# Performance work log

Measured on AMD Instinct MI355X. Metric: run time of the kernel, lower is better.

The kernel has to match this reference:

```python
import jax, jax.numpy as jnp
import numpy as np

BN_EPS = 1e-5
SG = jax.lax.stop_gradient


def _silu(z):
    return z * jax.nn.sigmoid(z)


def _binary_activation(x):
    # forward value = sign(x); backward goes through piecewise quadratic out3 (STE)
    out1 = jnp.where(x < -1, -1.0, x * x + 2 * x)
    out2 = jnp.where(x < 0, out1, -x * x + 2 * x)
    out3 = jnp.where(x < 1, out2, 1.0)
    return SG(jnp.sign(x)) - SG(out3) + out3


def _binarize_weight(w):
    # per-output-channel scaling factor * sign(w), STE through clipped weights
    sf = SG(jnp.mean(jnp.abs(w), axis=(1, 2, 3), keepdims=True))  # [O,1,1,1]
    cw = jnp.clip(w, -1.0, 1.0)
    return SG(sf * jnp.sign(w)) - SG(cw) + cw


def _conv3x3_s2(x, w, b):
    y = jax.lax.conv_general_dilated(
        x, w, window_strides=(2, 2), padding=((1, 1), (1, 1)),
        dimension_numbers=("NCHW", "OIHW", "NCHW"))
    return y + b[None, :, None, None]


def _batchnorm_train(x, gamma, beta):
    # training-mode BN: batch statistics over (N,H,W), biased variance
    mean = jnp.mean(x, axis=(0, 2, 3), keepdims=True)
    var = jnp.mean((x - mean) ** 2, axis=(0, 2, 3), keepdims=True)
    xhat = (x - mean) * jax.lax.rsqrt(var + BN_EPS)
    return xhat * gamma[None, :, None, None] + beta[None, :, None, None]


def _learnable_bias(x, emb, w, b):
    # bias = zero_module(linear)(SiLU(emb)) broadcast over H,W
    bias = _silu(emb) @ w.T + b  # [B, C]
    return x + bias[:, :, None, None]


def _avgpool2(x):
    B, C, H, W = x.shape
    return x.reshape(B, C, H // 2, 2, W // 2, 2).mean(axis=(3, 5))


def setup_inputs() -> dict:
    key = jax.random.key(0)
    ks = jax.random.split(key, 16)
    B, Cin, P, E, H, W = 32, 128, 256, 512, 64, 64
    scalor = P // Cin  # 2
    inp = {
        "x": jax.random.normal(ks[0], (B, Cin, H, W), jnp.float32),
        "emb": jax.random.normal(ks[1], (B, E), jnp.float32),
        "m1_w": jax.random.normal(ks[2], (Cin, E), jnp.float32) * 0.02,
        "m1_b": jnp.zeros((Cin,), jnp.float32),
        "conv_w": jax.random.uniform(ks[3], (scalor, Cin, Cin, 3, 3), jnp.float32, -1.0, 1.0) * 0.1,
        "conv_b": jax.random.normal(ks[4], (scalor, Cin), jnp.float32) * 0.01,
        "bn_g": jnp.ones((scalor, Cin), jnp.float32),
        "bn_b": jnp.zeros((scalor, Cin), jnp.float32),
        "m2_w": jax.random.normal(ks[5], (P, E), jnp.float32) * 0.02,
        "m2_b": jnp.zeros((P,), jnp.float32),
        "prelu_a": jnp.full((P,), 0.25, jnp.float32),
        "m3_w": jax.random.normal(ks[6], (P, E), jnp.float32) * 0.02,
        "m3_b": jnp.zeros((P,), jnp.float32),
    }
    return inp


def reference(x, emb, m1_w, m1_b, conv_w, conv_b, bn_g, bn_b,
              m2_w, m2_b, prelu_a, m3_w, m3_b):
    scalor = conv_w.shape[0]
    out = _learnable_bias(x, emb, m1_w, m1_b)
    out = _binary_activation(out)
    xp = _avgpool2(x)  # residual, [B,Cin,H/2,W/2]
    out_list = []
    for i in range(scalor):
        bw = _binarize_weight(conv_w[i])
        y = _conv3x3_s2(out, bw, conv_b[i])
        y = _batchnorm_train(y, bn_g[i], bn_b[i])
        out_list.append(y + xp)
    o = jnp.concatenate(out_list, axis=1)  # [B, planes, H/2, W/2]
    o = _learnable_bias(o, emb, m2_w, m2_b)
    a = prelu_a[None, :, None, None]
    o = jnp.where(o > 0, o, a * o)  # PReLU per channel
    o = _learnable_bias(o, emb, m3_w, m3_b)
    return o
```

## Files before the change

kernel.cpp:

```cpp
#include <hip/hip_runtime.h>
#include <cstdint>
#include <cstddef>

#define B_  32
#define CIN 128
#define P_  256
#define E_  512
#define H_  64
#define W_  64
#define HO  32
#define WO  32

__global__ void k_bw(const float* __restrict__ emb,
                     const float* __restrict__ m1_w, const float* __restrict__ m1_b,
                     const float* __restrict__ m2_w, const float* __restrict__ m2_b,
                     const float* __restrict__ m3_w, const float* __restrict__ m3_b,
                     const float* __restrict__ conv_w,
                     float* __restrict__ b1, float* __restrict__ b2, float* __restrict__ b3,
                     float* __restrict__ sf, unsigned int* __restrict__ wbits,
                     float* __restrict__ s1, float* __restrict__ s2) {
    int bid = blockIdx.x;
    int tid = threadIdx.x;
    int wave = tid >> 6, lane = tid & 63;

    if (bid < B_ * 160) {
        int n = bid / 160, rg = bid % 160;
        int row = rg * 4 + wave;
        const float* sp = emb + n * E_;
        const float* wrow; float bias; float* dst;
        if (row < CIN)            { wrow = m1_w + (size_t)row * E_;          bias = m1_b[row]; dst = b1 + n * CIN + row; }
        else if (row < CIN + P_)  { int c = row - CIN;      wrow = m2_w + (size_t)c * E_; bias = m2_b[c]; dst = b2 + n * P_ + c; }
        else                      { int c = row - CIN - P_; wrow = m3_w + (size_t)c * E_; bias = m3_b[c]; dst = b3 + n * P_ + c; }
        float acc = 0.f;
        #pragma unroll
        for (int j = 0; j < 8; j++) {
            int k = j * 64 + lane;
            float e = sp[k];
            acc += (e / (1.f + expf(-e))) * wrow[k];
        }
        #pragma unroll
        for (int off = 32; off > 0; off >>= 1) acc += __shfl_down(acc, off);
        if (lane == 0) *dst = acc + bias;
        return;
    }

    int base = (bid - B_ * 160) * 2;
    int oc = base + (wave >> 1);
    int iw = wave & 1;
    int i  = iw * 64 + lane;
    if (lane == 0 && iw == 0) { s1[oc] = 0.f; s2[oc] = 0.f; }
    const float* wp = conv_w + ((size_t)oc * CIN + i) * 9;
    float w[9]; float s = 0.f;
    #pragma unroll
    for (int t = 0; t < 9; t++) { w[t] = wp[t]; s += fabsf(w[t]); }
    #pragma unroll
    for (int t = 0; t < 9; t++) {
        unsigned long long m = __ballot(w[t] < 0.f);
        if (lane == 0) {
            wbits[oc * 36 + t * 4 + iw * 2 + 0] = (unsigned int)(m & 0xffffffffull);
            wbits[oc * 36 + t * 4 + iw * 2 + 1] = (unsigned int)(m >> 32);
        }
    }
    #pragma unroll
    for (int off = 32; off > 0; off >>= 1) s += __shfl_down(s, off);
    __shared__ float sred[4];
    if (lane == 0) sred[wave] = s;
    __syncthreads();
    if (tid == 0)        sf[base]     = (sred[0] + sred[1]) / 1152.f;
    else if (tid == 128) sf[base + 1] = (sred[2] + sred[3]) / 1152.f;
}

__global__ void k_prep(const float* __restrict__ x, const float* __restrict__ b1,
                       unsigned int* __restrict__ abits, float* __restrict__ xpool) {
    __shared__ float sb1[CIN];
    int n = blockIdx.x >> 5, h2 = blockIdx.x & 31;
    int tid = threadIdx.x;
    for (int i = tid; i < CIN; i += 256) sb1[i] = b1[n * CIN + i];
    __syncthreads();

    int pix = tid >> 1, half = tid & 1;
    int h = 2 * h2 + (pix >> 6), w = pix & 63;
    const float* xp = x + ((size_t)n * CIN + half * 64) * (H_ * W_) + (size_t)h * W_ + w;
    unsigned int wds[2];
    #pragma unroll
    for (int wd = 0; wd < 2; wd++) {
        unsigned int m = 0;
        #pragma unroll
        for (int b = 0; b < 32; b++) {
            float v = xp[(size_t)(wd * 32 + b) * (H_ * W_)] + sb1[half * 64 + wd * 32 + b];
            m |= (v < 0.f ? 1u : 0u) << b;
        }
        wds[wd] = m;
    }
    ((uint2*)abits)[((size_t)n * 4096 + (size_t)h * 64 + w) * 2 + half] = make_uint2(wds[0], wds[1]);

    for (int idx = tid; idx < CIN * WO; idx += 256) {
        int c = idx >> 5, w2 = idx & 31;
        const float* p = x + ((size_t)n * CIN + c) * (H_ * W_) + (size_t)(2 * h2) * W_ + 2 * w2;
        float2 a = *(const float2*)p;
        float2 b = *(const float2*)(p + W_);
        xpool[((size_t)n * CIN + c) * (HO * WO) + h2 * WO + w2] = 0.25f * (a.x + a.y + b.x + b.y);
    }
}

__global__ void __launch_bounds__(256, 4) k_convstat(const unsigned int* __restrict__ abits,
                                                     const unsigned int* __restrict__ wbits,
                                                     short* __restrict__ y16,
                                                     float* __restrict__ s1, float* __restrict__ s2) {
    __shared__ int red1[32][33], red2[32][33];
    int bid = blockIdx.x;
    int strip = bid & 3, ocg = (bid >> 2) & 7, n = bid >> 5;
    int tid = threadIdx.x;
    int wave = tid >> 6, lane = tid & 63;
    int oh = strip * 8 + (tid >> 5), ow = tid & 31;

    const uint4* asrc = ((const uint4*)abits) + ((size_t)n << 12);
    uint4 img[9]; int vmask = 0;
    #pragma unroll
    for (int kh = 0; kh < 3; kh++) {
        #pragma unroll
        for (int kw = 0; kw < 3; kw++) {
            int t = kh * 3 + kw;
            int r = 2 * oh - 1 + kh, c = 2 * ow - 1 + kw;
            bool v = (unsigned)r < 64u && (unsigned)c < 64u;
            img[t] = v ? asrc[r * 64 + c] : make_uint4(0u, 0u, 0u, 0u);
            vmask |= (v ? 1 : 0) << t;
        }
    }
    int base128 = 128 * __popc(vmask);

    const uint4* wp = ((const uint4*)wbits) + (size_t)ocg * 32 * 9;
    short* yp = y16 + (((size_t)n * P_ + ocg * 32) << 10) + strip * 256 + tid;
    #pragma unroll 4
    for (int o = 0; o < 32; o++) {
        int popsum = 0;
        #pragma unroll
        for (int t = 0; t < 9; t++) {
            uint4 a = img[t];
            uint4 w = wp[o * 9 + t];
            int p = __popc(a.x ^ w.x) + __popc(a.y ^ w.y) +
                    __popc(a.z ^ w.z) + __popc(a.w ^ w.w);
            popsum += ((vmask >> t) & 1) ? p : 0;
        }
        int s = base128 - 2 * popsum;
        yp[(size_t)o << 10] = (short)s;
        int vs = s, v2 = s * s;
        vs += __shfl_down(vs, 32); v2 += __shfl_down(v2, 32);
        vs += __shfl_down(vs, 16); v2 += __shfl_down(v2, 16);
        vs += __shfl_down(vs, 8);  v2 += __shfl_down(v2, 8);
        if (lane < 8) { red1[o][wave * 8 + lane] = vs; red2[o][wave * 8 + lane] = v2; }
    }
    __syncthreads();
    if (tid < 64) {
        int o = tid & 31;
        int a = 0;
        if (tid < 32) {
            #pragma unroll
            for (int p = 0; p < 32; p++) a += red1[o][p];
            atomicAdd(s1 + ocg * 32 + o, (float)a);
        } else {
            #pragma unroll
            for (int p = 0; p < 32; p++) a += red2[o][p];
            atomicAdd(s2 + ocg * 32 + o, (float)a);
        }
    }
}

__global__ void k_epi(const short* __restrict__ y16, const float* __restrict__ xpool,
                      const float* __restrict__ sf,
                      const float* __restrict__ s1, const float* __restrict__ s2,
                      const float* __restrict__ bn_g, const float* __restrict__ bn_b,
                      const float* __restrict__ b2, const float* __restrict__ b3,
                      const float* __restrict__ prelu_a, float* __restrict__ out) {
    int i4 = blockIdx.x * blockDim.x + threadIdx.x;
    int pix4 = i4 & 255;
    int c = (i4 >> 8) & 255;
    int n = i4 >> 16;
    short4 yv = ((const short4*)y16)[i4];
    float4 xv = ((const float4*)xpool)[((n * CIN + (c & 127)) << 8) + pix4];
    const float inv = 1.f / (B_ * HO * WO);
    float sc = sf[c];
    float m = sc * s1[c] * inv;
    float var = fmaf(-m, m, sc * sc * s2[c] * inv);
    float r = rsqrtf(var + 1e-5f) * bn_g[c];
    float add0 = bn_b[c] + b2[n * P_ + c];
    float a = prelu_a[c];
    float b3v = b3[n * P_ + c];
    float o0 = (sc * (float)yv.x - m) * r + add0 + xv.x; o0 = (o0 > 0.f ? o0 : a * o0) + b3v;
    float o1 = (sc * (float)yv.y - m) * r + add0 + xv.y; o1 = (o1 > 0.f ? o1 : a * o1) + b3v;
    float o2 = (sc * (float)yv.z - m) * r + add0 + xv.z; o2 = (o2 > 0.f ? o2 : a * o2) + b3v;
    float o3 = (sc * (float)yv.w - m) * r + add0 + xv.w; o3 = (o3 > 0.f ? o3 : a * o3) + b3v;
    ((float4*)out)[i4] = make_float4(o0, o1, o2, o3);
}

extern "C" void kernel_launch(void* const* d_in, const int* in_sizes, int n_in,
                              void* d_out, int out_size, void* d_ws, size_t ws_size,
                              hipStream_t stream) {
    const float* x      = (const float*)d_in[0];
    const float* emb    = (const float*)d_in[1];
    const float* m1_w   = (const float*)d_in[2];
    const float* m1_b   = (const float*)d_in[3];
    const float* conv_w = (const float*)d_in[4];
    const float* bn_g   = (const float*)d_in[6];
    const float* bn_b   = (const float*)d_in[7];
    const float* m2_w   = (const float*)d_in[8];
    const float* m2_b   = (const float*)d_in[9];
    const float* prelu_a= (const float*)d_in[10];
    const float* m3_w   = (const float*)d_in[11];
    const float* m3_b   = (const float*)d_in[12];

    float* out = (float*)d_out;

    float* wsf = (float*)d_ws;
    float* b1    = wsf;
    float* b2    = wsf + 4096;
    float* b3    = wsf + 12288;
    float* sf    = wsf + 20480;
    float* s1    = wsf + 20736;
    float* s2    = wsf + 20992;
    unsigned int* wbits = (unsigned int*)(wsf + 21248);
    unsigned int* abits = (unsigned int*)(wsf + 30464);
    float* xpool = wsf + 554752;
    short* y16   = (short*)(wsf + 4749056 + 16384);

    k_bw      <<<B_ * 160 + P_ / 2, 256, 0, stream>>>(emb, m1_w, m1_b, m2_w, m2_b, m3_w, m3_b,
                                                      conv_w, b1, b2, b3, sf, wbits, s1, s2);
    k_prep    <<<B_ * 32, 256, 0, stream>>>(x, b1, abits, xpool);
    k_convstat<<<B_ * 32, 256, 0, stream>>>(abits, wbits, y16, s1, s2);
    k_epi     <<<(B_ * P_ * HO * WO) / (4 * 256), 256, 0, stream>>>(y16, xpool, sf, s1, s2,
                                                                    bn_g, bn_b, b2, b3, prelu_a, out);
}
```

Baseline: 190.9 us.

## Pad binarized activation image and correct borders with precomputed weight sums

The packed activation bits are stored with a one-pixel zero border (pitch 65), so the XNOR-popcount conv loads its 3x3 taps without bounds checks or validity masks. Boundary outputs are fixed with per-channel corrections for the top row, left column and corner, computed in the weight-binarization kernel from sign counts. The conv kernel also launches twice as many blocks, each handling 16 output channels instead of 32, with a higher occupancy hint. This trades extra per-output correction loads and more atomics for less branch and select work in the inner loop and more parallelism.

```diff
diff --git a/kernel.cpp b/kernel.cpp
--- a/kernel.cpp
+++ b/kernel.cpp
@@ -11,6 +11,9 @@
 #define HO  32
 #define WO  32
 
+#define APITCH 65
+#define APIX   4225
+
 __global__ void k_bw(const float* __restrict__ emb,
                      const float* __restrict__ m1_w, const float* __restrict__ m1_b,
                      const float* __restrict__ m2_w, const float* __restrict__ m2_b,
@@ -18,6 +21,7 @@
                      const float* __restrict__ conv_w,
                      float* __restrict__ b1, float* __restrict__ b2, float* __restrict__ b3,
                      float* __restrict__ sf, unsigned int* __restrict__ wbits,
+                     int* __restrict__ cwrow, int* __restrict__ cwcol, int* __restrict__ cw0,
                      float* __restrict__ s1, float* __restrict__ s2) {
     int bid = blockIdx.x;
     int tid = threadIdx.x;
@@ -51,11 +55,13 @@
     if (lane == 0 && iw == 0) { s1[oc] = 0.f; s2[oc] = 0.f; }
     const float* wp = conv_w + ((size_t)oc * CIN + i) * 9;
     float w[9]; float s = 0.f;
+    int pc[9];
     #pragma unroll
     for (int t = 0; t < 9; t++) { w[t] = wp[t]; s += fabsf(w[t]); }
     #pragma unroll
     for (int t = 0; t < 9; t++) {
         unsigned long long m = __ballot(w[t] < 0.f);
+        pc[t] = __popcll(m);
         if (lane == 0) {
             wbits[oc * 36 + t * 4 + iw * 2 + 0] = (unsigned int)(m & 0xffffffffull);
             wbits[oc * 36 + t * 4 + iw * 2 + 1] = (unsigned int)(m >> 32);
@@ -64,10 +70,30 @@
     #pragma unroll
     for (int off = 32; off > 0; off >>= 1) s += __shfl_down(s, off);
     __shared__ float sred[4];
-    if (lane == 0) sred[wave] = s;
+    __shared__ int spc[4][9];
+    if (lane == 0) {
+        sred[wave] = s;
+        #pragma unroll
+        for (int t = 0; t < 9; t++) spc[wave][t] = pc[t];
+    }
     __syncthreads();
-    if (tid == 0)        sf[base]     = (sred[0] + sred[1]) / 1152.f;
-    else if (tid == 128) sf[base + 1] = (sred[2] + sred[3]) / 1152.f;
+    if (tid == 0) {
+        sf[base] = (sred[0] + sred[1]) / 1152.f;
+        int c_[9];
+        #pragma unroll
+        for (int t = 0; t < 9; t++) c_[t] = spc[0][t] + spc[1][t];
+        cwrow[base] = 384 - 2 * (c_[0] + c_[1] + c_[2]);
+        cwcol[base] = 384 - 2 * (c_[0] + c_[3] + c_[6]);
+        cw0[base]   = 128 - 2 * c_[0];
+    } else if (tid == 128) {
+        sf[base + 1] = (sred[2] + sred[3]) / 1152.f;
+        int c_[9];
+        #pragma unroll
+        for (int t = 0; t < 9; t++) c_[t] = spc[2][t] + spc[3][t];
+        cwrow[base + 1] = 384 - 2 * (c_[0] + c_[1] + c_[2]);
+        cwcol[base + 1] = 384 - 2 * (c_[0] + c_[3] + c_[6]);
+        cw0[base + 1]   = 128 - 2 * c_[0];
+    }
 }
 
 __global__ void k_prep(const float* __restrict__ x, const float* __restrict__ b1,
@@ -78,6 +104,14 @@
     for (int i = tid; i < CIN; i += 256) sb1[i] = b1[n * CIN + i];
     __syncthreads();
 
+    if (h2 == 0) {
+        for (int i = tid; i < 129; i += 256) {
+            size_t idx = (i < 65) ? ((size_t)n * APIX + i)
+                                  : ((size_t)n * APIX + (size_t)(i - 64) * APITCH);
+            ((uint4*)abits)[idx] = make_uint4(0u, 0u, 0u, 0u);
+        }
+    }
+
     int pix = tid >> 1, half = tid & 1;
     int h = 2 * h2 + (pix >> 6), w = pix & 63;
     const float* xp = x + ((size_t)n * CIN + half * 64) * (H_ * W_) + (size_t)h * W_ + w;
@@ -92,7 +126,8 @@
         }
         wds[wd] = m;
     }
-    ((uint2*)abits)[((size_t)n * 4096 + (size_t)h * 64 + w) * 2 + half] = make_uint2(wds[0], wds[1]);
+    ((uint2*)abits)[((size_t)n * APIX + (size_t)(h + 1) * APITCH + (w + 1)) * 2 + half] =
+        make_uint2(wds[0], wds[1]);
 
     for (int idx = tid; idx < CIN * WO; idx += 256) {
         int c = idx >> 5, w2 = idx & 31;
@@ -103,46 +138,48 @@
     }
 }
 
-__global__ void __launch_bounds__(256, 4) k_convstat(const unsigned int* __restrict__ abits,
+__global__ void __launch_bounds__(256, 6) k_convstat(const unsigned int* __restrict__ abits,
                                                      const unsigned int* __restrict__ wbits,
+                                                     const int* __restrict__ cwrow,
+                                                     const int* __restrict__ cwcol,
+                                                     const int* __restrict__ cw0,
                                                      short* __restrict__ y16,
                                                      float* __restrict__ s1, float* __restrict__ s2) {
-    __shared__ int red1[32][33], red2[32][33];
+    __shared__ int red1[16][33], red2[16][33];
     int bid = blockIdx.x;
-    int strip = bid & 3, ocg = (bid >> 2) & 7, n = bid >> 5;
+    int strip = bid & 3, og = (bid >> 2) & 15, n = bid >> 6;
     int tid = threadIdx.x;
     int wave = tid >> 6, lane = tid & 63;
     int oh = strip * 8 + (tid >> 5), ow = tid & 31;
-
-    const uint4* asrc = ((const uint4*)abits) + ((size_t)n << 12);
-    uint4 img[9]; int vmask = 0;
+    bool r0 = (oh == 0), c0 = (ow == 0);
+    bool rc0 = r0 && c0;
+
+    const uint4* asrc = ((const uint4*)abits) + (size_t)n * APIX;
+    uint4 img[9];
     #pragma unroll
     for (int kh = 0; kh < 3; kh++) {
         #pragma unroll
         for (int kw = 0; kw < 3; kw++) {
-            int t = kh * 3 + kw;
-            int r = 2 * oh - 1 + kh, c = 2 * ow - 1 + kw;
-            bool v = (unsigned)r < 64u && (unsigned)c < 64u;
-            img[t] = v ? asrc[r * 64 + c] : make_uint4(0u, 0u, 0u, 0u);
-            vmask |= (v ? 1 : 0) << t;
-        }
-    }
-    int base128 = 128 * __popc(vmask);
-
-    const uint4* wp = ((const uint4*)wbits) + (size_t)ocg * 32 * 9;
-    short* yp = y16 + (((size_t)n * P_ + ocg * 32) << 10) + strip * 256 + tid;
+            img[kh * 3 + kw] = asrc[(2 * oh + kh) * APITCH + (2 * ow + kw)];
+        }
+    }
+
+    int ocb = og * 16;
+    const uint4* wp = ((const uint4*)wbits) + (size_t)ocb * 9;
+    short* yp = y16 + (((size_t)n * P_ + ocb) << 10) + strip * 256 + tid;
     #pragma unroll 4
-    for (int o = 0; o < 32; o++) {
+    for (int o = 0; o < 16; o++) {
         int popsum = 0;
         #pragma unroll
         for (int t = 0; t < 9; t++) {
             uint4 a = img[t];
             uint4 w = wp[o * 9 + t];
-            int p = __popc(a.x ^ w.x) + __popc(a.y ^ w.y) +
-                    __popc(a.z ^ w.z) + __popc(a.w ^ w.w);
-            popsum += ((vmask >> t) & 1) ? p : 0;
-        }
-        int s = base128 - 2 * popsum;
+            popsum += __popc(a.x ^ w.x) + __popc(a.y ^ w.y) +
+                      __popc(a.z ^ w.z) + __popc(a.w ^ w.w);
+        }
+        int srow = cwrow[ocb + o], scol = cwcol[ocb + o], sz = cw0[ocb + o];
+        int corr = (r0 ? srow : 0) + (c0 ? scol : 0) - (rc0 ? sz : 0);
+        int s = 1152 - 2 * popsum - corr;
         yp[(size_t)o << 10] = (short)s;
         int vs = s, v2 = s * s;
         vs += __shfl_down(vs, 32); v2 += __shfl_down(v2, 32);
@@ -151,17 +188,17 @@
         if (lane < 8) { red1[o][wave * 8 + lane] = vs; red2[o][wave * 8 + lane] = v2; }
     }
     __syncthreads();
-    if (tid < 64) {
-        int o = tid & 31;
+    if (tid < 32) {
+        int o = tid & 15;
         int a = 0;
-        if (tid < 32) {
+        if (tid < 16) {
             #pragma unroll
             for (int p = 0; p < 32; p++) a += red1[o][p];
-            atomicAdd(s1 + ocg * 32 + o, (float)a);
+            atomicAdd(s1 + ocb + o, (float)a);
         } else {
             #pragma unroll
             for (int p = 0; p < 32; p++) a += red2[o][p];
-            atomicAdd(s2 + ocg * 32 + o, (float)a);
+            atomicAdd(s2 + ocb + o, (float)a);
         }
     }
 }
@@ -219,14 +256,18 @@
     float* s1    = wsf + 20736;
     float* s2    = wsf + 20992;
     unsigned int* wbits = (unsigned int*)(wsf + 21248);
-    unsigned int* abits = (unsigned int*)(wsf + 30464);
-    float* xpool = wsf + 554752;
-    short* y16   = (short*)(wsf + 4749056 + 16384);
+    int* cwrow = (int*)(wsf + 30464);
+    int* cwcol = (int*)(wsf + 30720);
+    int* cw0   = (int*)(wsf + 30976);
+    unsigned int* abits = (unsigned int*)(wsf + 31232);
+    float* xpool = wsf + 572032;
+    short* y16   = (short*)(wsf + 4766336);
 
     k_bw      <<<B_ * 160 + P_ / 2, 256, 0, stream>>>(emb, m1_w, m1_b, m2_w, m2_b, m3_w, m3_b,
-                                                      conv_w, b1, b2, b3, sf, wbits, s1, s2);
+                                                      conv_w, b1, b2, b3, sf, wbits,
+                                                      cwrow, cwcol, cw0, s1, s2);
     k_prep    <<<B_ * 32, 256, 0, stream>>>(x, b1, abits, xpool);
-    k_convstat<<<B_ * 32, 256, 0, stream>>>(abits, wbits, y16, s1, s2);
+    k_convstat<<<B_ * 64, 256, 0, stream>>>(abits, wbits, cwrow, cwcol, cw0, y16, s1, s2);
     k_epi     <<<(B_ * P_ * HO * WO) / (4 * 256), 256, 0, stream>>>(y16, xpool, sf, s1, s2,
                                                                     bn_g, bn_b, b2, b3, prelu_a, out);
 }
```

Measured after the change: 186.9 us. -2.1%, faster.
